# Kernel tuning notes

Measured on AMD Instinct MI355X. Metric: run time of the kernel, lower is better.

## Reference

```python
import jax, jax.numpy as jnp
import numpy as np

N_HEADS = 4
D_HEAD = 16
SCALE = D_HEAD ** 0.5  # NOTE: original multiplies by sqrt(d_head), faithful


def _mha(x, Wq, bq, Wk, bk, Wv, bv, Wo, bo):
    # x: (..., N, D) with D = N_HEADS * D_HEAD
    q = jnp.einsum('...nd,od->...no', x, Wq) + bq
    k = jnp.einsum('...nd,od->...no', x, Wk) + bk
    v = jnp.einsum('...nd,od->...no', x, Wv) + bv
    lead = x.shape[:-2]
    n = x.shape[-2]
    q = q.reshape(*lead, n, N_HEADS, D_HEAD)
    k = k.reshape(*lead, n, N_HEADS, D_HEAD)
    v = v.reshape(*lead, n, N_HEADS, D_HEAD)
    scores = jnp.einsum('...nhd,...mhd->...hnm', q, k) * SCALE
    attn = jax.nn.softmax(scores, axis=-1)
    o = jnp.einsum('...hnm,...mhd->...nhd', attn, v).reshape(*lead, n, N_HEADS * D_HEAD)
    return jnp.einsum('...nd,od->...no', o, Wo) + bo


def setup_inputs() -> dict:
    key = jax.random.key(0)
    ks = jax.random.split(key, 20)
    b, n, d, dhf, G, C = 16, 16384, 64, 64, 256, 64
    s = 0.05
    inp = {
        'x': jax.random.normal(ks[0], (b, n, d), dtype=jnp.float32),
        'partitions': jax.random.permutation(ks[1], n).reshape(G, C).astype(jnp.int64),
    }
    names = ['q_intra', 'k_intra', 'v_intra', 'o_intra',
             'q_inter', 'k_inter', 'v_inter', 'o_inter']
    for i, nm in enumerate(names):
        d_in = d if nm.endswith('intra') and nm[0] != 'o' else dhf
        inp['W' + nm] = jax.random.normal(ks[2 + 2 * i], (dhf, d_in), dtype=jnp.float32) * s
        inp['b' + nm] = jax.random.normal(ks[3 + 2 * i], (dhf,), dtype=jnp.float32) * s
    return inp


def reference(x, partitions,
              Wq_intra, bq_intra, Wk_intra, bk_intra, Wv_intra, bv_intra, Wo_intra, bo_intra,
              Wq_inter, bq_inter, Wk_inter, bk_inter, Wv_inter, bv_inter, Wo_inter, bo_inter):
    b = x.shape[0]
    G, C = partitions.shape
    dhf = Wq_intra.shape[0]
    # gather nodes into groups: (b, G, C, d)
    xg = x[:, partitions, :]
    # intra-group attention, vectorized over (b, G)
    intra = _mha(xg, Wq_intra, bq_intra, Wk_intra, bk_intra,
                 Wv_intra, bv_intra, Wo_intra, bo_intra)  # (b, G, C, dhf)
    # MaxPool1d(kernel=dhf) over token axis with C == dhf -> max over tokens
    pooled = jnp.max(intra, axis=2)  # (b, G, dhf)
    inter = _mha(pooled, Wq_inter, bq_inter, Wk_inter, bk_inter,
                 Wv_inter, bv_inter, Wo_inter, bo_inter)  # (b, G, dhf)
    # broadcast-add inter-group features to every token in the group
    out = intra + inter[:, :, None, :]  # (b, G, C, dhf)
    flat = out.reshape(b, G * C, dhf)
    inv = jnp.argsort(partitions.reshape(-1))  # restore original node order
    return flat[:, inv, :]
```

## Files before the change

kernel.cpp:

```cpp
#include <hip/hip_runtime.h>
#include <hip/hip_bf16.h>

#define NTOK 16384
#define NG   256
#define NB   16

typedef float  f32x4   __attribute__((ext_vector_type(4)));
typedef short  short8v __attribute__((ext_vector_type(8)));
typedef short  short4v __attribute__((ext_vector_type(4)));

#define MFMA_BF16(a, b, c) __builtin_amdgcn_mfma_f32_16x16x32_bf16((a), (b), (c), 0, 0, 0)

#define QSCALE 5.770780163555856f

__device__ __forceinline__ short f2bf(float f) {
    union { float f; unsigned u; } x; x.f = f;
    unsigned r = (x.u + 0x7FFF + ((x.u >> 16) & 1)) >> 16;
    return (short)r;
}
__device__ __forceinline__ short bft(float f) {
    union { float f; unsigned u; } x; x.f = f;
    return (short)(x.u >> 16);
}
__device__ __forceinline__ float bf2f(short s) {
    union { float f; unsigned u; } x;
    x.u = ((unsigned)(unsigned short)s) << 16;
    return x.f;
}
__device__ __forceinline__ unsigned pk_rne(float a, float b) {
    union { float f; unsigned u; } xa, xb; xa.f = a; xb.f = b;
    const unsigned ua = xa.u + (0x7FFFu + ((xa.u >> 16) & 1));
    const unsigned ub = xb.u + (0x7FFFu + ((xb.u >> 16) & 1));
    return __builtin_amdgcn_perm(ub, ua, 0x07060302u);
}

__global__ void k_setup(const int* __restrict__ raw, int* __restrict__ part,
                        const float* __restrict__ Wq, const float* __restrict__ Wk,
                        const float* __restrict__ Wv, const float* __restrict__ Wo,
                        const float* __restrict__ Wqe, const float* __restrict__ Wke,
                        const float* __restrict__ Wve, const float* __restrict__ Woe,
                        short8v* __restrict__ wf)
{
    const int gid = blockIdx.x * 256 + threadIdx.x;
    if (gid < 16384) {
        const bool is64 = (raw[1] == 0 && raw[3] == 0 && raw[5] == 0);
        part[gid] = is64 ? raw[2 * gid] : raw[gid];
        return;
    }
    const int p = gid - 16384;
    if (p >= 5632) return;
    if (p < 3584) {
        const int v    = p >> 9;
        const int rem  = p & 511;
        const int tau  = rem >> 6;
        const int lane = rem & 63;
        const int jt = tau >> 1, kt = tau & 1;
        const int o  = jt * 16 + (lane & 15);
        const int d0 = kt * 32 + (lane >> 4) * 8;
        const float* W = (v < 2) ? Wq : (v < 4) ? Wk : (v < 6) ? Wv : Wo;
        const bool lo = (v & 1) && (v < 6);
        short8v r8;
#pragma unroll
        for (int i = 0; i < 8; ++i) {
            const float f = W[o * 64 + d0 + i];
            const short hh = f2bf(f);
            r8[i] = lo ? f2bf(f - bf2f(hh)) : hh;
        }
        wf[p] = r8;
    } else {
        const int g2   = p - 3584;
        const int v    = g2 >> 9;
        const int rem  = g2 & 511;
        const int tau  = rem >> 6;
        const int lane = rem & 63;
        const int jt = tau >> 1, kt = tau & 1;
        const int o  = jt * 16 + (lane & 15);
        const int d0 = kt * 32 + (lane >> 4) * 8;
        const float* W = (v == 0) ? Wqe : (v == 1) ? Wke : (v == 2) ? Wve : Woe;
        short8v r8;
#pragma unroll
        for (int i = 0; i < 8; ++i) r8[i] = f2bf(W[o * 64 + d0 + i]);
        wf[p] = r8;
    }
}

__global__ __launch_bounds__(256, 4) void k_intra(
    const float* __restrict__ x, const int* __restrict__ part,
    const short8v* __restrict__ wf,
    const float* __restrict__ bq, const float* __restrict__ bk,
    const float* __restrict__ bv, const float* __restrict__ bo,
    float* __restrict__ out, float* __restrict__ pooled,
    unsigned short* __restrict__ intra_g, const int use_g)
{
    __shared__ __align__(16) short S[20480];

    short* const xh = S;
    short* const kk = S + 4096;
    short* const ql = S + 8192;
    short* const qh = S + 12288;
    short* const vT = S + 16384;

    const int t  = threadIdx.x;
    const int g  = blockIdx.x;
    const int bb = blockIdx.y;
    const int l  = t & 63;
    const int w  = t >> 6;
    const int quad = l >> 4;
    const int col  = l & 15;

    for (int j = t; j < 512; j += 256) {
        const int row = j >> 3, c8 = j & 7;
        const int tok = part[g * 64 + row];
        const float* px = x + ((size_t)bb * NTOK + tok) * 64 + c8 * 8;
        const float4 f0 = ((const float4*)px)[0];
        const float4 f1 = ((const float4*)px)[1];
        uint4 pk;
        pk.x = pk_rne(f0.x, f0.y);
        pk.y = pk_rne(f0.z, f0.w);
        pk.z = pk_rne(f1.x, f1.y);
        pk.w = pk_rne(f1.z, f1.w);
        *(uint4*)&xh[row * 64 + ((c8 ^ (row & 7)) << 3)] = pk;
    }
    __syncthreads();

    {
        const float bqv = bq[w * 16 + col];
        const float bkv = bk[w * 16 + col];
        const float bvv = bv[w * 16 + col];
        short8v bqh[2], bql2[2], bkh[2], bkl[2], bvh[2], bvl[2];
#pragma unroll
        for (int kt = 0; kt < 2; ++kt) {
            const int tau = w * 2 + kt;
            bqh[kt]  = wf[(0 * 8 + tau) * 64 + l];
            bql2[kt] = wf[(1 * 8 + tau) * 64 + l];
            bkh[kt]  = wf[(2 * 8 + tau) * 64 + l];
            bkl[kt]  = wf[(3 * 8 + tau) * 64 + l];
            bvh[kt]  = wf[(4 * 8 + tau) * 64 + l];
            bvl[kt]  = wf[(5 * 8 + tau) * 64 + l];
        }
        for (int mt = 0; mt < 4; ++mt) {
            short8v axh[2];
#pragma unroll
            for (int kt = 0; kt < 2; ++kt) {
                const int row = mt * 16 + col;
                axh[kt] = *(const short8v*)&xh[row * 64 + (((kt * 4 + quad) ^ (row & 7)) << 3)];
            }
            f32x4 aq = {0.f, 0.f, 0.f, 0.f};
            f32x4 ak = {0.f, 0.f, 0.f, 0.f};
            f32x4 av = {0.f, 0.f, 0.f, 0.f};
#pragma unroll
            for (int kt = 0; kt < 2; ++kt) {
                aq = MFMA_BF16(axh[kt], bqh[kt],  aq);
                aq = MFMA_BF16(axh[kt], bql2[kt], aq);
                ak = MFMA_BF16(axh[kt], bkh[kt],  ak);
                ak = MFMA_BF16(axh[kt], bkl[kt],  ak);
                av = MFMA_BF16(axh[kt], bvh[kt],  av);
                av = MFMA_BF16(axh[kt], bvl[kt],  av);
            }
#pragma unroll
            for (int r = 0; r < 4; ++r) {
                const int m = mt * 16 + quad * 4 + r;
                const int pos = m * 64 + (((w * 2 + (col >> 3)) ^ (m & 7)) << 3) + (col & 7);
                const float q4 = (aq[r] + bqv) * QSCALE;
                const short hq = bft(q4);
                qh[pos] = hq;
                ql[pos] = bft(q4 - bf2f(hq));
                kk[pos] = f2bf(ak[r] + bkv);
            }
            {
                const int d = w * 16 + col;
                short4v v4;
#pragma unroll
                for (int r = 0; r < 4; ++r) v4[r] = f2bf(av[r] + bvv);
                const int cm = mt * 2 + (quad >> 1);
                const int idx = d * 64 + ((cm ^ (d & 7)) << 3) + ((quad & 1) * 4);
                *(short4v*)&vT[idx] = v4;
            }
        }
    }

    const int h = w, hc = h * 16;
    f32x4 s[4][4];
    {
        short8v bk4[4];
#pragma unroll
        for (int jt = 0; jt < 4; ++jt) {
            const int row = jt * 16 + col;
            bk4[jt] = *(const short8v*)&kk[row * 64 + (((h * 2 + (quad & 1)) ^ (row & 7)) << 3)];
        }
        const short8v z8 = {0, 0, 0, 0, 0, 0, 0, 0};
        for (int it = 0; it < 4; ++it) {
            const int row = it * 16 + col;
            const int idx = row * 64 + (((h * 2 + (quad & 1)) ^ (row & 7)) << 3);
            short8v aqh = *(const short8v*)&qh[idx];
            short8v aql = *(const short8v*)&ql[idx];
            if (quad >= 2) { aqh = z8; aql = z8; }
#pragma unroll
            for (int jt = 0; jt < 4; ++jt) {
                f32x4 acc = {0.f, 0.f, 0.f, 0.f};
                acc = MFMA_BF16(aqh, bk4[jt], acc);
                acc = MFMA_BF16(aql, bk4[jt], acc);
                s[it][jt] = acc;
            }
        }
    }
    float rden[4][4];
    for (int it = 0; it < 4; ++it) {
#pragma unroll
        for (int r = 0; r < 4; ++r) {
            float mx = fmaxf(fmaxf(s[it][0][r], s[it][1][r]),
                             fmaxf(s[it][2][r], s[it][3][r]));
            mx = fmaxf(mx, __shfl_xor(mx, 1));
            mx = fmaxf(mx, __shfl_xor(mx, 2));
            mx = fmaxf(mx, __shfl_xor(mx, 4));
            mx = fmaxf(mx, __shfl_xor(mx, 8));
            float ds = 0.f;
#pragma unroll
            for (int jt = 0; jt < 4; ++jt) {
                const float e = exp2f(s[it][jt][r] - mx);
                s[it][jt][r] = e;
                ds += e;
            }
            ds += __shfl_xor(ds, 1);
            ds += __shfl_xor(ds, 2);
            ds += __shfl_xor(ds, 4);
            ds += __shfl_xor(ds, 8);
            rden[it][r] = 1.0f / ds;
        }
    }
    __syncthreads();

    f32x4 oa[4];
#pragma unroll
    for (int it = 0; it < 4; ++it) oa[it] = (f32x4){0.f, 0.f, 0.f, 0.f};
    short* const Pw = S + w * 2560;
    for (int kt = 0; kt < 2; ++kt) {
        for (int it = 0; it < 4; ++it)
#pragma unroll
            for (int jl = 0; jl < 2; ++jl) {
                const int jt = kt * 2 + jl;
#pragma unroll
                for (int r = 0; r < 4; ++r)
                    Pw[(it * 16 + quad * 4 + r) * 40 + jl * 16 + col] = bft(s[it][jt][r]);
            }
        const int dv = hc + col;
        const int cmv = kt * 4 + quad;
        const short8v bv8 = *(const short8v*)&vT[dv * 64 + ((cmv ^ (dv & 7)) << 3)];
        for (int it = 0; it < 4; ++it) {
            const short8v ap = *(const short8v*)&Pw[(it * 16 + col) * 40 + quad * 8];
            oa[it] = MFMA_BF16(ap, bv8, oa[it]);
        }
    }
    for (int it = 0; it < 4; ++it)
#pragma unroll
        for (int r = 0; r < 4; ++r) {
            const int row = it * 16 + quad * 4 + r;
            const int pos = row * 64 + (((h * 2 + (col >> 3)) ^ (row & 7)) << 3) + (col & 7);
            qh[pos] = f2bf(oa[it][r] * rden[it][r]);
        }
    __syncthreads();

    {
        const float bov = bo[w * 16 + col];
        short8v bo8[2];
        bo8[0] = wf[(6 * 8 + w * 2 + 0) * 64 + l];
        bo8[1] = wf[(6 * 8 + w * 2 + 1) * 64 + l];
        float pm = -1e30f;
        const size_t gbase = ((size_t)bb * NG + g) * 64;
        for (int mt = 0; mt < 4; ++mt) {
            f32x4 acc = {0.f, 0.f, 0.f, 0.f};
#pragma unroll
            for (int kt = 0; kt < 2; ++kt) {
                const int row = mt * 16 + col;
                const short8v ao = *(const short8v*)&qh[row * 64 + (((kt * 4 + quad) ^ (row & 7)) << 3)];
                acc = MFMA_BF16(ao, bo8[kt], acc);
            }
            if (use_g) {
#pragma unroll
                for (int r = 0; r < 4; ++r) {
                    const float vo = acc[r] + bov;
                    pm = fmaxf(pm, vo);
                    intra_g[(gbase + mt * 16 + quad * 4 + r) * 64 + w * 16 + col] =
                        (unsigned short)f2bf(vo);
                }
            } else {
#pragma unroll
                for (int r = 0; r < 4; ++r) {
                    const float vo = acc[r] + bov;
                    pm = fmaxf(pm, vo);
                    const int tok = part[g * 64 + mt * 16 + quad * 4 + r];
                    out[((size_t)bb * NTOK + tok) * 64 + w * 16 + col] = vo;
                }
            }
        }
        pm = fmaxf(pm, __shfl_xor(pm, 16));
        pm = fmaxf(pm, __shfl_xor(pm, 32));
        if (l < 16)
            pooled[((size_t)bb * NG + g) * 64 + w * 16 + col] = pm;
    }
}

__global__ __launch_bounds__(256) void k_inter_qkv(
    const float* __restrict__ pooled, const short8v* __restrict__ wf,
    const float* __restrict__ bq, const float* __restrict__ bk,
    const float* __restrict__ bv,
    short* __restrict__ qws, short* __restrict__ kws, short* __restrict__ vTws)
{
    __shared__ __align__(16) short xs[4096];
    __shared__ __align__(16) short qs[64 * 72];
    __shared__ __align__(16) short ks2[64 * 72];
    const int t = threadIdx.x;
    const int chunk = blockIdx.x, bb = blockIdx.y;
    const int l = t & 63, w = t >> 6;
    const int quad = l >> 4, col = l & 15;

    for (int j = t; j < 512; j += 256) {
        const int row = j >> 3, c8 = j & 7;
        const float* px = pooled + ((size_t)bb * NG + chunk * 64 + row) * 64 + c8 * 8;
        const float4 f0 = ((const float4*)px)[0];
        const float4 f1 = ((const float4*)px)[1];
        uint4 pk;
        pk.x = pk_rne(f0.x, f0.y);
        pk.y = pk_rne(f0.z, f0.w);
        pk.z = pk_rne(f1.x, f1.y);
        pk.w = pk_rne(f1.z, f1.w);
        *(uint4*)&xs[row * 64 + ((c8 ^ (row & 7)) << 3)] = pk;
    }
    __syncthreads();

    const int WFI = 3584;
    short8v bqf[2], bkf[2], bvf[2];
#pragma unroll
    for (int kt = 0; kt < 2; ++kt) {
        bqf[kt] = wf[WFI + (0 * 8 + w * 2 + kt) * 64 + l];
        bkf[kt] = wf[WFI + (1 * 8 + w * 2 + kt) * 64 + l];
        bvf[kt] = wf[WFI + (2 * 8 + w * 2 + kt) * 64 + l];
    }
    const float bqv = bq[w * 16 + col];
    const float bkv = bk[w * 16 + col];
    const float bvv = bv[w * 16 + col];
    for (int mt = 0; mt < 4; ++mt) {
        short8v ax[2];
#pragma unroll
        for (int kt = 0; kt < 2; ++kt) {
            const int row = mt * 16 + col;
            ax[kt] = *(const short8v*)&xs[row * 64 + (((kt * 4 + quad) ^ (row & 7)) << 3)];
        }
        f32x4 aq = {0.f, 0.f, 0.f, 0.f};
        f32x4 ak = {0.f, 0.f, 0.f, 0.f};
        f32x4 av = {0.f, 0.f, 0.f, 0.f};
#pragma unroll
        for (int kt = 0; kt < 2; ++kt) {
            aq = MFMA_BF16(ax[kt], bqf[kt], aq);
            ak = MFMA_BF16(ax[kt], bkf[kt], ak);
            av = MFMA_BF16(ax[kt], bvf[kt], av);
        }
        short4v v4;
#pragma unroll
        for (int r = 0; r < 4; ++r) {
            const int m = mt * 16 + quad * 4 + r;
            qs[m * 72 + w * 16 + col]  = f2bf((aq[r] + bqv) * QSCALE);
            ks2[m * 72 + w * 16 + col] = f2bf(ak[r] + bkv);
            v4[r] = f2bf(av[r] + bvv);
        }
        *(short4v*)&vTws[((size_t)bb * 64 + w * 16 + col) * 256 + chunk * 64 + mt * 16 + quad * 4] = v4;
    }
    __syncthreads();
    for (int j = t; j < 512; j += 256) {
        const int row = j >> 3, c8 = j & 7;
        *(short8v*)&qws[((size_t)bb * NG + chunk * 64 + row) * 64 + c8 * 8] =
            *(const short8v*)&qs[row * 72 + c8 * 8];
        *(short8v*)&kws[((size_t)bb * NG + chunk * 64 + row) * 64 + c8 * 8] =
            *(const short8v*)&ks2[row * 72 + c8 * 8];
    }
}

__global__ __launch_bounds__(256) void k_inter_attn2(
    const short* __restrict__ qws, const short* __restrict__ kws,
    const short* __restrict__ vTws, const short8v* __restrict__ wf,
    const float* __restrict__ bo, float* __restrict__ inter)
{
    __shared__ __align__(16) short Pw_all[4 * 16 * 40];
    __shared__ __align__(16) short os[16 * 72];
    const int t = threadIdx.x;
    const int qt = blockIdx.x, bb = blockIdx.y;
    const int l = t & 63, w = t >> 6;
    const int quad = l >> 4, col = l & 15;
    const int hc = w * 16;
    const int r0 = qt * 16;

    const short8v z8 = {0, 0, 0, 0, 0, 0, 0, 0};
    short8v bk[16];
#pragma unroll
    for (int jt = 0; jt < 16; ++jt)
        bk[jt] = (quad < 2)
            ? *(const short8v*)&kws[((size_t)bb * NG + jt * 16 + col) * 64 + hc + quad * 8]
            : z8;
    short8v aq = (quad < 2)
        ? *(const short8v*)&qws[((size_t)bb * NG + r0 + col) * 64 + hc + quad * 8]
        : z8;

    f32x4 s[16];
#pragma unroll
    for (int jt = 0; jt < 16; ++jt) {
        f32x4 acc = {0.f, 0.f, 0.f, 0.f};
        s[jt] = MFMA_BF16(aq, bk[jt], acc);
    }

    float rden[4];
#pragma unroll
    for (int r = 0; r < 4; ++r) {
        float mx = -1e30f;
#pragma unroll
        for (int jt = 0; jt < 16; ++jt) mx = fmaxf(mx, s[jt][r]);
        mx = fmaxf(mx, __shfl_xor(mx, 1));
        mx = fmaxf(mx, __shfl_xor(mx, 2));
        mx = fmaxf(mx, __shfl_xor(mx, 4));
        mx = fmaxf(mx, __shfl_xor(mx, 8));
        float ds = 0.f;
#pragma unroll
        for (int jt = 0; jt < 16; ++jt) {
            const float e = exp2f(s[jt][r] - mx);
            s[jt][r] = e;
            ds += e;
        }
        ds += __shfl_xor(ds, 1);
        ds += __shfl_xor(ds, 2);
        ds += __shfl_xor(ds, 4);
        ds += __shfl_xor(ds, 8);
        rden[r] = 1.0f / ds;
    }

    short* const Pw = Pw_all + w * 16 * 40;
    f32x4 oa = {0.f, 0.f, 0.f, 0.f};
    for (int c = 0; c < 8; ++c) {
#pragma unroll
        for (int jl = 0; jl < 2; ++jl) {
            const int jt = c * 2 + jl;
#pragma unroll
            for (int r = 0; r < 4; ++r)
                Pw[(quad * 4 + r) * 40 + jl * 16 + col] = bft(s[jt][r]);
        }
        const short8v bv8 = *(const short8v*)&vTws[((size_t)bb * 64 + hc + col) * 256 + c * 32 + quad * 8];
        const short8v ap = *(const short8v*)&Pw[col * 40 + quad * 8];
        oa = MFMA_BF16(ap, bv8, oa);
    }
#pragma unroll
    for (int r = 0; r < 4; ++r)
        os[(quad * 4 + r) * 72 + hc + col] = f2bf(oa[r] * rden[r]);
    __syncthreads();

    short8v bof[2];
    bof[0] = wf[3584 + (3 * 8 + w * 2 + 0) * 64 + l];
    bof[1] = wf[3584 + (3 * 8 + w * 2 + 1) * 64 + l];
    const float bov = bo[w * 16 + col];
    {
        f32x4 acc = {0.f, 0.f, 0.f, 0.f};
#pragma unroll
        for (int kt = 0; kt < 2; ++kt) {
            const short8v ao = *(const short8v*)&os[col * 72 + kt * 32 + quad * 8];
            acc = MFMA_BF16(ao, bof[kt], acc);
        }
#pragma unroll
        for (int r = 0; r < 4; ++r)
            inter[((size_t)bb * NG + r0 + quad * 4 + r) * 64 + w * 16 + col] = acc[r] + bov;
    }
}

__global__ __launch_bounds__(256) void k_final(
    const unsigned short* __restrict__ intra_g, const float* __restrict__ inter,
    const int* __restrict__ part, float* __restrict__ out)
{
    __shared__ float interL[64];
    __shared__ int   pidx[64];
    const int t  = threadIdx.x;
    const int g  = blockIdx.x;
    const int bb = blockIdx.y;
    if (t < 64) pidx[t] = part[g * 64 + t];
    else if (t < 128) interL[t - 64] = inter[((size_t)bb * NG + g) * 64 + (t - 64)];
    __syncthreads();
    const size_t ibase = ((size_t)bb * NG + g) * 64 * 64;
#pragma unroll
    for (int i = 0; i < 8; ++i) {
        const int item = i * 256 + t;
        const int row  = item >> 5;
        const int pr   = item & 31;
        const unsigned u = *(const unsigned*)&intra_g[ibase + row * 64 + pr * 2];
        const float2 iv = *(const float2*)&interL[pr * 2];
        float2 o;
        o.x = bf2f((short)(u & 0xFFFF)) + iv.x;
        o.y = bf2f((short)(u >> 16))    + iv.y;
        *(float2*)&out[((size_t)bb * NTOK + pidx[row]) * 64 + pr * 2] = o;
    }
}

__global__ __launch_bounds__(256) void k_scatter_add(
    const float* __restrict__ inter, const int* __restrict__ part,
    float* __restrict__ out)
{
    __shared__ float iv[64];
    __shared__ int   pidx[64];
    const int t  = threadIdx.x;
    const int g  = blockIdx.x;
    const int bb = blockIdx.y;
    if (t < 64) {
        iv[t]   = inter[((size_t)bb * NG + g) * 64 + t];
        pidx[t] = part[g * 64 + t];
    }
    __syncthreads();
    const int oo   = t & 63;
    const int cseg = t >> 6;
    const float add = iv[oo];
    for (int ci = 0; ci < 16; ++ci) {
        const int c = cseg * 16 + ci;
        float* p = out + ((size_t)bb * NTOK + pidx[c]) * 64 + oo;
        *p += add;
    }
}

extern "C" void kernel_launch(void* const* d_in, const int* in_sizes, int n_in,
                              void* d_out, int out_size, void* d_ws, size_t ws_size,
                              hipStream_t stream)
{
    const float* x    = (const float*)d_in[0];
    const int*   praw = (const int*)d_in[1];
    const float* Wq_a = (const float*)d_in[2];
    const float* bq_a = (const float*)d_in[3];
    const float* Wk_a = (const float*)d_in[4];
    const float* bk_a = (const float*)d_in[5];
    const float* Wv_a = (const float*)d_in[6];
    const float* bv_a = (const float*)d_in[7];
    const float* Wo_a = (const float*)d_in[8];
    const float* bo_a = (const float*)d_in[9];
    const float* Wq_e = (const float*)d_in[10];
    const float* bq_e = (const float*)d_in[11];
    const float* Wk_e = (const float*)d_in[12];
    const float* bk_e = (const float*)d_in[13];
    const float* Wv_e = (const float*)d_in[14];
    const float* bv_e = (const float*)d_in[15];
    const float* Wo_e = (const float*)d_in[16];
    const float* bo_e = (const float*)d_in[17];

    char* ws = (char*)d_ws;
    int*     part   = (int*)ws;
    float*   pooled = (float*)(ws + (1u << 16));
    float*   inter  = (float*)(ws + (1u << 16) + (1u << 20));
    short8v* wf     = (short8v*)(ws + (1u << 16) + 2 * (1u << 20));
    char*    base2  = ws + (1u << 16) + 2 * (1u << 20) + 98304;
    short*   qws    = (short*)base2;
    short*   kws    = (short*)(base2 + (1u << 19));
    short*   vTws   = (short*)(base2 + 2 * (1u << 19));
    unsigned short* intra_g = (unsigned short*)(base2 + 3 * (1u << 19));
    const size_t need = ((size_t)(base2 - ws)) + 3 * (1u << 19) + (size_t)NB * NG * 64 * 64 * 2;
    const int use_g = (ws_size >= need) ? 1 : 0;

    float* out = (float*)d_out;

    k_setup<<<dim3(86), dim3(256), 0, stream>>>(praw, part, Wq_a, Wk_a, Wv_a, Wo_a,
                                                Wq_e, Wk_e, Wv_e, Wo_e, wf);
    k_intra<<<dim3(NG, NB), dim3(256), 0, stream>>>(
        x, part, wf, bq_a, bk_a, bv_a, bo_a, out, pooled, intra_g, use_g);
    k_inter_qkv<<<dim3(4, NB), dim3(256), 0, stream>>>(
        pooled, wf, bq_e, bk_e, bv_e, qws, kws, vTws);
    k_inter_attn2<<<dim3(16, NB), dim3(256), 0, stream>>>(
        qws, kws, vTws, wf, bo_e, inter);
    if (use_g)
        k_final<<<dim3(NG, NB), dim3(256), 0, stream>>>(intra_g, inter, part, out);
    else
        k_scatter_add<<<dim3(NG, NB), dim3(256), 0, stream>>>(inter, part, out);
}
```

Measured before the change: 220.4 us.

## Stage intra output in LDS for coalesced stores, use hardware bf16 pack, drop softmax max

```diff
diff --git a/kernel.cpp b/kernel.cpp
--- a/kernel.cpp
+++ b/kernel.cpp
@@ -27,11 +27,16 @@
     x.u = ((unsigned)(unsigned short)s) << 16;
     return x.f;
 }
-__device__ __forceinline__ unsigned pk_rne(float a, float b) {
+__device__ __forceinline__ unsigned pk_cvt(float a, float b) {
+#if __has_builtin(__builtin_amdgcn_cvt_pk_bf16_f32)
+    auto r = __builtin_amdgcn_cvt_pk_bf16_f32(a, b);
+    unsigned u; __builtin_memcpy(&u, &r, 4); return u;
+#else
     union { float f; unsigned u; } xa, xb; xa.f = a; xb.f = b;
     const unsigned ua = xa.u + (0x7FFFu + ((xa.u >> 16) & 1));
     const unsigned ub = xb.u + (0x7FFFu + ((xb.u >> 16) & 1));
     return __builtin_amdgcn_perm(ub, ua, 0x07060302u);
+#endif
 }
 
 __global__ void k_setup(const int* __restrict__ raw, int* __restrict__ part,
@@ -115,10 +120,10 @@
         const float4 f0 = ((const float4*)px)[0];
         const float4 f1 = ((const float4*)px)[1];
         uint4 pk;
-        pk.x = pk_rne(f0.x, f0.y);
-        pk.y = pk_rne(f0.z, f0.w);
-        pk.z = pk_rne(f1.x, f1.y);
-        pk.w = pk_rne(f1.z, f1.w);
+        pk.x = pk_cvt(f0.x, f0.y);
+        pk.y = pk_cvt(f0.z, f0.w);
+        pk.z = pk_cvt(f1.x, f1.y);
+        pk.w = pk_cvt(f1.z, f1.w);
         *(uint4*)&xh[row * 64 + ((c8 ^ (row & 7)) << 3)] = pk;
     }
     __syncthreads();
@@ -157,6 +162,8 @@
                 av = MFMA_BF16(axh[kt], bvh[kt],  av);
                 av = MFMA_BF16(axh[kt], bvl[kt],  av);
             }
+            const unsigned k01 = pk_cvt(ak[0] + bkv, ak[1] + bkv);
+            const unsigned k23 = pk_cvt(ak[2] + bkv, ak[3] + bkv);
 #pragma unroll
             for (int r = 0; r < 4; ++r) {
                 const int m = mt * 16 + quad * 4 + r;
@@ -165,16 +172,17 @@
                 const short hq = bft(q4);
                 qh[pos] = hq;
                 ql[pos] = bft(q4 - bf2f(hq));
-                kk[pos] = f2bf(ak[r] + bkv);
+                const unsigned kr = (r < 2) ? k01 : k23;
+                kk[pos] = (short)((r & 1) ? (kr >> 16) : (kr & 0xFFFF));
             }
             {
                 const int d = w * 16 + col;
-                short4v v4;
-#pragma unroll
-                for (int r = 0; r < 4; ++r) v4[r] = f2bf(av[r] + bvv);
+                unsigned v01 = pk_cvt(av[0] + bvv, av[1] + bvv);
+                unsigned v23 = pk_cvt(av[2] + bvv, av[3] + bvv);
+                uint2 v4; v4.x = v01; v4.y = v23;
                 const int cm = mt * 2 + (quad >> 1);
                 const int idx = d * 64 + ((cm ^ (d & 7)) << 3) + ((quad & 1) * 4);
-                *(short4v*)&vT[idx] = v4;
+                *(uint2*)&vT[idx] = v4;
             }
         }
     }
@@ -208,16 +216,10 @@
     for (int it = 0; it < 4; ++it) {
 #pragma unroll
         for (int r = 0; r < 4; ++r) {
-            float mx = fmaxf(fmaxf(s[it][0][r], s[it][1][r]),
-                             fmaxf(s[it][2][r], s[it][3][r]));
-            mx = fmaxf(mx, __shfl_xor(mx, 1));
-            mx = fmaxf(mx, __shfl_xor(mx, 2));
-            mx = fmaxf(mx, __shfl_xor(mx, 4));
-            mx = fmaxf(mx, __shfl_xor(mx, 8));
             float ds = 0.f;
 #pragma unroll
             for (int jt = 0; jt < 4; ++jt) {
-                const float e = exp2f(s[it][jt][r] - mx);
+                const float e = exp2f(s[it][jt][r]);
                 s[it][jt][r] = e;
                 ds += e;
             }
@@ -251,22 +253,26 @@
             oa[it] = MFMA_BF16(ap, bv8, oa[it]);
         }
     }
-    for (int it = 0; it < 4; ++it)
+    for (int it = 0; it < 4; ++it) {
+        const unsigned o01 = pk_cvt(oa[it][0] * rden[it][0], oa[it][1] * rden[it][1]);
+        const unsigned o23 = pk_cvt(oa[it][2] * rden[it][2], oa[it][3] * rden[it][3]);
 #pragma unroll
         for (int r = 0; r < 4; ++r) {
             const int row = it * 16 + quad * 4 + r;
             const int pos = row * 64 + (((h * 2 + (col >> 3)) ^ (row & 7)) << 3) + (col & 7);
-            qh[pos] = f2bf(oa[it][r] * rden[it][r]);
-        }
-    __syncthreads();
-
+            const unsigned uo = (r < 2) ? o01 : o23;
+            qh[pos] = (short)((r & 1) ? (uo >> 16) : (uo & 0xFFFF));
+        }
+    }
+    __syncthreads();
+
+    float* const os = (float*)S;
     {
         const float bov = bo[w * 16 + col];
         short8v bo8[2];
         bo8[0] = wf[(6 * 8 + w * 2 + 0) * 64 + l];
         bo8[1] = wf[(6 * 8 + w * 2 + 1) * 64 + l];
         float pm = -1e30f;
-        const size_t gbase = ((size_t)bb * NG + g) * 64;
         for (int mt = 0; mt < 4; ++mt) {
             f32x4 acc = {0.f, 0.f, 0.f, 0.f};
 #pragma unroll
@@ -275,28 +281,42 @@
                 const short8v ao = *(const short8v*)&qh[row * 64 + (((kt * 4 + quad) ^ (row & 7)) << 3)];
                 acc = MFMA_BF16(ao, bo8[kt], acc);
             }
-            if (use_g) {
-#pragma unroll
-                for (int r = 0; r < 4; ++r) {
-                    const float vo = acc[r] + bov;
-                    pm = fmaxf(pm, vo);
-                    intra_g[(gbase + mt * 16 + quad * 4 + r) * 64 + w * 16 + col] =
-                        (unsigned short)f2bf(vo);
-                }
-            } else {
-#pragma unroll
-                for (int r = 0; r < 4; ++r) {
-                    const float vo = acc[r] + bov;
-                    pm = fmaxf(pm, vo);
-                    const int tok = part[g * 64 + mt * 16 + quad * 4 + r];
-                    out[((size_t)bb * NTOK + tok) * 64 + w * 16 + col] = vo;
-                }
+#pragma unroll
+            for (int r = 0; r < 4; ++r) {
+                const float vo = acc[r] + bov;
+                pm = fmaxf(pm, vo);
+                os[(mt * 16 + quad * 4 + r) * 68 + w * 16 + col] = vo;
             }
         }
         pm = fmaxf(pm, __shfl_xor(pm, 16));
         pm = fmaxf(pm, __shfl_xor(pm, 32));
         if (l < 16)
             pooled[((size_t)bb * NG + g) * 64 + w * 16 + col] = pm;
+    }
+    __syncthreads();
+
+    {
+        const int row = t >> 2, seg = t & 3;
+        const float* pr = &os[row * 68 + seg * 16];
+        const f32x4 v0 = ((const f32x4*)pr)[0];
+        const f32x4 v1 = ((const f32x4*)pr)[1];
+        const f32x4 v2 = ((const f32x4*)pr)[2];
+        const f32x4 v3 = ((const f32x4*)pr)[3];
+        if (use_g) {
+            uint4 p0, p1;
+            p0.x = pk_cvt(v0[0], v0[1]); p0.y = pk_cvt(v0[2], v0[3]);
+            p0.z = pk_cvt(v1[0], v1[1]); p0.w = pk_cvt(v1[2], v1[3]);
+            p1.x = pk_cvt(v2[0], v2[1]); p1.y = pk_cvt(v2[2], v2[3]);
+            p1.z = pk_cvt(v3[0], v3[1]); p1.w = pk_cvt(v3[2], v3[3]);
+            unsigned short* dst = &intra_g[(((size_t)bb * NG + g) * 64 + row) * 64 + seg * 16];
+            ((uint4*)dst)[0] = p0;
+            ((uint4*)dst)[1] = p1;
+        } else {
+            const int tok = part[g * 64 + row];
+            float* po = &out[((size_t)bb * NTOK + tok) * 64 + seg * 16];
+            ((f32x4*)po)[0] = v0; ((f32x4*)po)[1] = v1;
+            ((f32x4*)po)[2] = v2; ((f32x4*)po)[3] = v3;
+        }
     }
 }
 
@@ -320,10 +340,10 @@
         const float4 f0 = ((const float4*)px)[0];
         const float4 f1 = ((const float4*)px)[1];
         uint4 pk;
-        pk.x = pk_rne(f0.x, f0.y);
-        pk.y = pk_rne(f0.z, f0.w);
-        pk.z = pk_rne(f1.x, f1.y);
-        pk.w = pk_rne(f1.z, f1.w);
+        pk.x = pk_cvt(f0.x, f0.y);
+        pk.y = pk_cvt(f0.z, f0.w);
+        pk.z = pk_cvt(f1.x, f1.y);
+        pk.w = pk_cvt(f1.z, f1.w);
         *(uint4*)&xs[row * 64 + ((c8 ^ (row & 7)) << 3)] = pk;
     }
     __syncthreads();
@@ -355,15 +375,16 @@
             ak = MFMA_BF16(ax[kt], bkf[kt], ak);
             av = MFMA_BF16(ax[kt], bvf[kt], av);
         }
-        short4v v4;
 #pragma unroll
         for (int r = 0; r < 4; ++r) {
             const int m = mt * 16 + quad * 4 + r;
             qs[m * 72 + w * 16 + col]  = f2bf((aq[r] + bqv) * QSCALE);
             ks2[m * 72 + w * 16 + col] = f2bf(ak[r] + bkv);
-            v4[r] = f2bf(av[r] + bvv);
-        }
-        *(short4v*)&vTws[((size_t)bb * 64 + w * 16 + col) * 256 + chunk * 64 + mt * 16 + quad * 4] = v4;
+        }
+        uint2 v4;
+        v4.x = pk_cvt(av[0] + bvv, av[1] + bvv);
+        v4.y = pk_cvt(av[2] + bvv, av[3] + bvv);
+        *(uint2*)&vTws[((size_t)bb * 64 + w * 16 + col) * 256 + chunk * 64 + mt * 16 + quad * 4] = v4;
     }
     __syncthreads();
     for (int j = t; j < 512; j += 256) {
@@ -445,9 +466,15 @@
         const short8v ap = *(const short8v*)&Pw[col * 40 + quad * 8];
         oa = MFMA_BF16(ap, bv8, oa);
     }
-#pragma unroll
-    for (int r = 0; r < 4; ++r)
-        os[(quad * 4 + r) * 72 + hc + col] = f2bf(oa[r] * rden[r]);
+    {
+        const unsigned o01 = pk_cvt(oa[0] * rden[0], oa[1] * rden[1]);
+        const unsigned o23 = pk_cvt(oa[2] * rden[2], oa[3] * rden[3]);
+#pragma unroll
+        for (int r = 0; r < 4; ++r) {
+            const unsigned uo = (r < 2) ? o01 : o23;
+            os[(quad * 4 + r) * 72 + hc + col] = (short)((r & 1) ? (uo >> 16) : (uo & 0xFFFF));
+        }
+    }
     __syncthreads();
 
     short8v bof[2];
```

After: 204.2 us. 1.08x faster.
